# Performance work log

Measured on AMD Instinct MI355X. Metric: run time of the kernel, lower is better.

The kernel has to match this reference:

```python
import jax, jax.numpy as jnp
import numpy as np

B, T, D, H = 8, 512, 1024, 16
DH = D // H  # per-head feature dim (64)


def setup_inputs() -> dict:
    key = jax.random.key(0)
    ks = jax.random.split(key, 10)
    s = 1.0 / np.sqrt(DH)
    inp = {
        "X_data": jax.random.normal(ks[0], (B, T, D), dtype=jnp.float32),
        "mask": jnp.ones((B, T), dtype=jnp.int32),
        # per-head Q/K/V projections (each SelfAttention has its own d_h x d_h weights)
        "Wq": jax.random.normal(ks[1], (H, DH, DH), dtype=jnp.float32) * s,
        "bq": jnp.zeros((H, DH), dtype=jnp.float32),
        "Wk": jax.random.normal(ks[2], (H, DH, DH), dtype=jnp.float32) * s,
        "bk": jnp.zeros((H, DH), dtype=jnp.float32),
        "Wv": jax.random.normal(ks[3], (H, DH, DH), dtype=jnp.float32) * s,
        "bv": jnp.zeros((H, DH), dtype=jnp.float32),
        # AttentionFusion: linear on concatenated head outputs -> len_feature_new
        "Wf": jax.random.normal(ks[4], (D, D), dtype=jnp.float32) * (1.0 / np.sqrt(D)),
        "bf": jnp.zeros((D,), dtype=jnp.float32),
    }
    return inp


def reference(X_data, mask, Wq, bq, Wk, bk, Wv, bv, Wf, bf):
    # Split features into heads: [B, T, H, DH] (equal partitions since D % H == 0)
    Xh = X_data.reshape(B, T, H, DH)
    # Batched per-head projections (replaces the Python loop over heads)
    Q = jnp.einsum("bthd,hde->bhte", Xh, Wq) + bq[None, :, None, :]
    K = jnp.einsum("bthd,hde->bhte", Xh, Wk) + bk[None, :, None, :]
    V = jnp.einsum("bthd,hde->bhte", Xh, Wv) + bv[None, :, None, :]
    scale = 1.0 / jnp.sqrt(jnp.asarray(DH, dtype=Q.dtype))
    scores = jnp.einsum("bhqe,bhke->bhqk", Q, K) * scale  # [B, H, T, T]
    scores = jnp.where(mask[:, None, None, :] > 0, scores, jnp.asarray(-1e9, scores.dtype))
    att = jax.nn.softmax(scores, axis=-1)
    out = jnp.einsum("bhqk,bhke->bhqe", att, V)  # [B, H, T, DH]
    # Concatenate heads (same order as the per-head loop) and fuse
    out = out.transpose(0, 2, 1, 3).reshape(B, T, D)
    fused = out @ Wf + bf  # AttentionFusion linear
    return fused
```

## Files before the change

### kernel.cpp

```cpp
#include <hip/hip_runtime.h>
#include <math.h>

#define B 8
#define T 512
#define D 1024
#define H 16
#define DH 64

typedef __bf16 bf16;
typedef __attribute__((ext_vector_type(8))) __bf16 bf16x8;
typedef __attribute__((ext_vector_type(4))) __bf16 bf16x4;
typedef __attribute__((ext_vector_type(4))) float f32x4;

__device__ __forceinline__ void gld16(const void* g, void* l) {
    __builtin_amdgcn_global_load_lds(
        (const __attribute__((address_space(1))) void*)g,
        (__attribute__((address_space(3))) void*)l, 16, 0, 0);
}


__global__ __launch_bounds__(256) void prep_w(
    const float* __restrict__ Wq, const float* __restrict__ Wk,
    const float* __restrict__ Wv, const float* __restrict__ Wf,
    bf16* __restrict__ WqT, bf16* __restrict__ WkT,
    bf16* __restrict__ WvT, bf16* __restrict__ WfT)
{
    __shared__ bf16 Ts[64 * 72];
    const int blk = blockIdx.x, tid = threadIdx.x;
    if (blk < 48) {
        const int m = blk >> 4, h = blk & 15;
        const float* src = (m == 0 ? Wq : (m == 1 ? Wk : Wv)) + h * 4096;
        bf16* dst = (m == 0 ? WqT : (m == 1 ? WkT : WvT)) + h * 4096;
        for (int i = tid; i < 1024; i += 256) {
            const int d = i >> 4, eq = (i & 15) * 4;
            const float4 w = *(const float4*)(src + d * 64 + eq);
            Ts[(eq + 0) * 72 + d] = (bf16)w.x; Ts[(eq + 1) * 72 + d] = (bf16)w.y;
            Ts[(eq + 2) * 72 + d] = (bf16)w.z; Ts[(eq + 3) * 72 + d] = (bf16)w.w;
        }
        __syncthreads();
        for (int i = tid; i < 512; i += 256) {
            const int e = i >> 3, kc = (i & 7) * 8;
            *(bf16x8*)(dst + e * 64 + kc) = *(const bf16x8*)&Ts[e * 72 + kc];
        }
    } else {
        const int ti = blk - 48, k0 = (ti >> 4) * 64, n0 = (ti & 15) * 64;
        for (int i = tid; i < 1024; i += 256) {
            const int k = i >> 4, nq = (i & 15) * 4;
            const float4 w = *(const float4*)(Wf + (size_t)(k0 + k) * D + n0 + nq);
            Ts[(nq + 0) * 72 + k] = (bf16)w.x; Ts[(nq + 1) * 72 + k] = (bf16)w.y;
            Ts[(nq + 2) * 72 + k] = (bf16)w.z; Ts[(nq + 3) * 72 + k] = (bf16)w.w;
        }
        __syncthreads();
        for (int i = tid; i < 512; i += 256) {
            const int n = i >> 3, kc = (i & 7) * 8;
            *(bf16x8*)(WfT + (size_t)(n0 + n) * D + k0 + kc) = *(const bf16x8*)&Ts[n * 72 + kc];
        }
    }
}

__global__ __launch_bounds__(256) void qkv_mfma(
    const float* __restrict__ X,
    const bf16* __restrict__ WqT, const bf16* __restrict__ WkT,
    const bf16* __restrict__ WvT,
    const float* __restrict__ bq, const float* __restrict__ bk,
    const float* __restrict__ bv,
    bf16* __restrict__ Qb, bf16* __restrict__ Kb, bf16* __restrict__ Vtb)
{
    __shared__ bf16 Xs[128 * 64];
    __shared__ bf16 Wqs[64 * 64], Wks[64 * 64], Wvs[64 * 64];
    __shared__ bf16 Stage[128 * 76];

    const int bh = blockIdx.x & 127, t0 = (blockIdx.x >> 7) * 128;
    const int b = bh >> 4, h = bh & 15;
    const int tid = threadIdx.x, wave = tid >> 6, lane = tid & 63;
    const int quad = lane >> 4, l15 = lane & 15;
    const int lr = lane >> 3, lc = lane & 7;
    const int csw = (lc ^ lr) * 8;

    for (int i = tid; i < 1024; i += 256) {
        const int row = i >> 3, c = i & 7;
        const float* src = X + (size_t)(b * T + t0 + row) * D + h * DH + c * 8;
        const float4 x0 = *(const float4*)src;
        const float4 x1 = *(const float4*)(src + 4);
        bf16x8 t;
        t[0] = (bf16)x0.x; t[1] = (bf16)x0.y; t[2] = (bf16)x0.z; t[3] = (bf16)x0.w;
        t[4] = (bf16)x1.x; t[5] = (bf16)x1.y; t[6] = (bf16)x1.z; t[7] = (bf16)x1.w;
        *(bf16x8*)&Xs[row * 64 + (c ^ (row & 7)) * 8] = t;
    }
    {
        const int r1 = wave * 16;
#pragma unroll
        for (int j = 0; j < 2; ++j) {
            gld16(WqT + (size_t)h * 4096 + (r1 + j * 8 + lr) * 64 + csw, &Wqs[(r1 + j * 8) * 64]);
            gld16(WkT + (size_t)h * 4096 + (r1 + j * 8 + lr) * 64 + csw, &Wks[(r1 + j * 8) * 64]);
            gld16(WvT + (size_t)h * 4096 + (r1 + j * 8 + lr) * 64 + csw, &Wvs[(r1 + j * 8) * 64]);
        }
    }
    __syncthreads();

    bf16x8 af[2][2];
#pragma unroll
    for (int mt = 0; mt < 2; ++mt)
#pragma unroll
        for (int ks = 0; ks < 2; ++ks) {
            const int row = wave * 32 + mt * 16 + l15;
            af[mt][ks] = *(const bf16x8*)&Xs[row * 64 + ((ks * 4 + quad) ^ (l15 & 7)) * 8];
        }

    auto compute = [&](const bf16* Bmat, f32x4 acc[2][4]) {
#pragma unroll
        for (int ks = 0; ks < 2; ++ks) {
            bf16x8 bfr[4];
#pragma unroll
            for (int nt = 0; nt < 4; ++nt)
                bfr[nt] = *(const bf16x8*)&Bmat[(nt * 16 + l15) * 64 + ((ks * 4 + quad) ^ (l15 & 7)) * 8];
#pragma unroll
            for (int mt = 0; mt < 2; ++mt)
#pragma unroll
                for (int nt = 0; nt < 4; ++nt)
                    acc[mt][nt] = __builtin_amdgcn_mfma_f32_16x16x32_bf16(
                        af[mt][ks], bfr[nt], acc[mt][nt], 0, 0, 0);
        }
    };

    const size_t bhTD = (size_t)bh * T * DH;

    {
        f32x4 acc[2][4] = {};
        compute(Wqs, acc);
#pragma unroll
        for (int mt = 0; mt < 2; ++mt)
#pragma unroll
            for (int nt = 0; nt < 4; ++nt) {
                const float bias = bq[h * DH + nt * 16 + l15];
#pragma unroll
                for (int reg = 0; reg < 4; ++reg)
                    Stage[(wave * 32 + mt * 16 + quad * 4 + reg) * 76 + nt * 16 + l15] =
                        (bf16)((acc[mt][nt][reg] + bias) * 0.125f);
            }
        __syncthreads();
        for (int i = tid; i < 1024; i += 256) {
            const int row = i >> 3, c = (i & 7) * 8;
            *(bf16x8*)(Qb + bhTD + (size_t)(t0 + row) * DH + c) = *(const bf16x8*)&Stage[row * 76 + c];
        }
        __syncthreads();
    }
    {
        f32x4 acc[2][4] = {};
        compute(Wks, acc);
#pragma unroll
        for (int mt = 0; mt < 2; ++mt)
#pragma unroll
            for (int nt = 0; nt < 4; ++nt) {
                const float bias = bk[h * DH + nt * 16 + l15];
#pragma unroll
                for (int reg = 0; reg < 4; ++reg)
                    Stage[(wave * 32 + mt * 16 + quad * 4 + reg) * 76 + nt * 16 + l15] =
                        (bf16)(acc[mt][nt][reg] + bias);
            }
        __syncthreads();
        for (int i = tid; i < 1024; i += 256) {
            const int row = i >> 3, c = (i & 7) * 8;
            *(bf16x8*)(Kb + bhTD + (size_t)(t0 + row) * DH + c) = *(const bf16x8*)&Stage[row * 76 + c];
        }
        __syncthreads();
    }
    {
        f32x4 acc[2][4] = {};
        compute(Wvs, acc);
#pragma unroll
        for (int mt = 0; mt < 2; ++mt)
#pragma unroll
            for (int nt = 0; nt < 4; ++nt) {
                const int e = nt * 16 + l15;
                const float bias = bv[h * DH + e];
#pragma unroll
                for (int reg = 0; reg < 4; ++reg) {
                    const int tl = wave * 32 + mt * 16 + quad * 4 + reg;
                    Stage[e * 152 + tl] = (bf16)(acc[mt][nt][reg] + bias);
                }
            }
        __syncthreads();
        for (int i = tid; i < 1024; i += 256) {
            const int e = i >> 4, c = (i & 15) * 8;
            *(bf16x8*)(Vtb + (size_t)bh * DH * T + (size_t)e * T + t0 + c) =
                *(const bf16x8*)&Stage[e * 152 + c];
        }
    }
}

__global__ __launch_bounds__(256) void attn_mfma(
    const bf16* __restrict__ Qb, const bf16* __restrict__ Kb,
    const bf16* __restrict__ Vtb, const int* __restrict__ mask,
    bf16* __restrict__ Ob)
{
    __shared__ bf16 Ks[128 * 64];
    __shared__ bf16 Vts[64 * 128];
    __shared__ bf16 Pl[4][32 * 136];
    __shared__ int msk[128];

    const int bh = blockIdx.x & 127, q0 = (blockIdx.x >> 7) * 128;
    const int b = bh >> 4, h = bh & 15;
    const int tid = threadIdx.x, wave = tid >> 6, lane = tid & 63;
    const int quad = lane >> 4, l15 = lane & 15;
    const int lr = lane >> 3, lc = lane & 7;
    const int csw = (lc ^ lr) * 8;

    const size_t bhTD = (size_t)bh * T * DH;
    const size_t bhDT = (size_t)bh * DH * T;

    bf16x8 qf[2][2];
#pragma unroll
    for (int mt = 0; mt < 2; ++mt)
#pragma unroll
        for (int ks = 0; ks < 2; ++ks)
            qf[mt][ks] = *(const bf16x8*)(Qb + bhTD +
                (size_t)(q0 + wave * 32 + mt * 16 + l15) * DH + ks * 32 + quad * 8);

    f32x4 acc[2][4] = {};
    float lst[2][4] = {};

    for (int kt = 0; kt < 4; ++kt) {
        const int k0 = kt * 128;
        __syncthreads();
        {
            const int r0 = wave * 32;
#pragma unroll
            for (int j = 0; j < 4; ++j)
                gld16(Kb + bhTD + (size_t)(k0 + r0 + j * 8 + lr) * DH + csw,
                      &Ks[(r0 + j * 8) * 64]);
            const int e0 = wave * 16;
#pragma unroll
            for (int j = 0; j < 4; ++j) {
                const int er = j * 4 + (lane >> 4);
                const int csw2 = ((lane & 15) ^ er) * 8;
                gld16(Vtb + bhDT + (size_t)(e0 + er) * T + k0 + csw2,
                      &Vts[(e0 + j * 4) * 128]);
            }
            if (tid < 128) msk[tid] = mask[(size_t)b * T + k0 + tid];
        }
        __syncthreads();

#pragma unroll
        for (int nt = 0; nt < 8; ++nt) {
            const int krow = nt * 16 + l15;
            const bf16x8 kf0 = *(const bf16x8*)&Ks[krow * 64 + ((quad) ^ (l15 & 7)) * 8];
            const bf16x8 kf1 = *(const bf16x8*)&Ks[krow * 64 + ((4 + quad) ^ (l15 & 7)) * 8];
            const int mv = msk[krow];
#pragma unroll
            for (int mt = 0; mt < 2; ++mt) {
                f32x4 s = {};
                s = __builtin_amdgcn_mfma_f32_16x16x32_bf16(qf[mt][0], kf0, s, 0, 0, 0);
                s = __builtin_amdgcn_mfma_f32_16x16x32_bf16(qf[mt][1], kf1, s, 0, 0, 0);
#pragma unroll
                for (int reg = 0; reg < 4; ++reg) {
                    const float p = (mv > 0) ? __expf(s[reg]) : 0.f;
                    lst[mt][reg] += p;
                    Pl[wave][(mt * 16 + quad * 4 + reg) * 136 + nt * 16 + l15] = (bf16)p;
                }
            }
        }
        __builtin_amdgcn_wave_barrier();

#pragma unroll
        for (int kc = 0; kc < 4; ++kc) {
            const bf16x8 pf0 = *(const bf16x8*)&Pl[wave][(l15) * 136 + kc * 32 + quad * 8];
            const bf16x8 pf1 = *(const bf16x8*)&Pl[wave][(16 + l15) * 136 + kc * 32 + quad * 8];
#pragma unroll
            for (int nt = 0; nt < 4; ++nt) {
                const int erow = nt * 16 + l15;
                const bf16x8 vf = *(const bf16x8*)&Vts[erow * 128 + ((kc * 4 + quad) ^ (l15 & 15)) * 8];
                acc[0][nt] = __builtin_amdgcn_mfma_f32_16x16x32_bf16(pf0, vf, acc[0][nt], 0, 0, 0);
                acc[1][nt] = __builtin_amdgcn_mfma_f32_16x16x32_bf16(pf1, vf, acc[1][nt], 0, 0, 0);
            }
        }
    }

    __syncthreads();
    bf16* Ostage = &Pl[0][0];
#pragma unroll
    for (int mt = 0; mt < 2; ++mt)
#pragma unroll
        for (int reg = 0; reg < 4; ++reg) {
            float l = lst[mt][reg];
            l += __shfl_xor(l, 1);
            l += __shfl_xor(l, 2);
            l += __shfl_xor(l, 4);
            l += __shfl_xor(l, 8);
            const float inv = 1.f / l;
            const int row = wave * 32 + mt * 16 + quad * 4 + reg;
#pragma unroll
            for (int nt = 0; nt < 4; ++nt)
                Ostage[row * 76 + nt * 16 + l15] = (bf16)(acc[mt][nt][reg] * inv);
        }
    __syncthreads();
    for (int i = tid; i < 1024; i += 256) {
        const int row = i >> 3, c = (i & 7) * 8;
        *(bf16x8*)(Ob + ((size_t)b * T + q0 + row) * D + h * DH + c) =
            *(const bf16x8*)&Ostage[row * 76 + c];
    }
}

__global__ __launch_bounds__(256) void fuse_mfma(
    const bf16* __restrict__ Ob, const bf16* __restrict__ WfT,
    const float* __restrict__ bfv, float* __restrict__ out)
{
    __shared__ bf16 smem[128 * 128 + 64 * 128];
    bf16* As = smem;
    bf16* Bs = smem + 128 * 128;

    const int col0 = blockIdx.x * 64;
    const int row0 = blockIdx.y * 128;
    const int tid = threadIdx.x, wave = tid >> 6, lane = tid & 63;
    const int quad = lane >> 4, l15 = lane & 15;
    const int lr4 = lane >> 4, lc16 = lane & 15;
    const int wm = wave * 32;

    f32x4 acc[2][4] = {};

    for (int k0 = 0; k0 < D; k0 += 128) {
        __syncthreads();
#pragma unroll
        for (int j = 0; j < 8; ++j) {
            const int row = wm + j * 4 + lr4;
            gld16(Ob + (size_t)(row0 + row) * D + k0 + ((lc16 ^ (row & 15)) * 8),
                  &As[(wm + j * 4) * 128]);
        }
#pragma unroll
        for (int j = 0; j < 4; ++j) {
            const int row = wave * 16 + j * 4 + lr4;
            gld16(WfT + (size_t)(col0 + row) * D + k0 + ((lc16 ^ (row & 15)) * 8),
                  &Bs[(wave * 16 + j * 4) * 128]);
        }
        __syncthreads();
#pragma unroll
        for (int ks = 0; ks < 4; ++ks) {
            bf16x8 af[2], bfr[4];
#pragma unroll
            for (int mt = 0; mt < 2; ++mt) {
                const int row = wm + mt * 16 + l15;
                af[mt] = *(const bf16x8*)&As[row * 128 + ((ks * 4 + quad) ^ l15) * 8];
            }
#pragma unroll
            for (int nt = 0; nt < 4; ++nt)
                bfr[nt] = *(const bf16x8*)&Bs[(nt * 16 + l15) * 128 + ((ks * 4 + quad) ^ l15) * 8];
#pragma unroll
            for (int mt = 0; mt < 2; ++mt)
#pragma unroll
                for (int nt = 0; nt < 4; ++nt)
                    acc[mt][nt] = __builtin_amdgcn_mfma_f32_16x16x32_bf16(af[mt], bfr[nt], acc[mt][nt], 0, 0, 0);
        }
    }

    __syncthreads();
    float* Ofs = (float*)smem;
    float bias[4];
#pragma unroll
    for (int nt = 0; nt < 4; ++nt) bias[nt] = bfv[col0 + nt * 16 + l15];
#pragma unroll
    for (int mt = 0; mt < 2; ++mt)
#pragma unroll
        for (int reg = 0; reg < 4; ++reg) {
            const int row = wm + mt * 16 + quad * 4 + reg;
#pragma unroll
            for (int nt = 0; nt < 4; ++nt)
                Ofs[row * 68 + nt * 16 + l15] = acc[mt][nt][reg] + bias[nt];
        }
    __syncthreads();
    for (int i = tid; i < 2048; i += 256) {
        const int row = i >> 4, c = (i & 15) * 4;
        *(float4*)(out + (size_t)(row0 + row) * D + col0 + c) = *(const float4*)&Ofs[row * 68 + c];
    }
}

extern "C" void kernel_launch(void* const* d_in, const int* in_sizes, int n_in,
                              void* d_out, int out_size, void* d_ws, size_t ws_size,
                              hipStream_t stream) {
    const float* X   = (const float*)d_in[0];
    const int* mask  = (const int*)d_in[1];
    const float* Wq  = (const float*)d_in[2];
    const float* bq  = (const float*)d_in[3];
    const float* Wk  = (const float*)d_in[4];
    const float* bk  = (const float*)d_in[5];
    const float* Wv  = (const float*)d_in[6];
    const float* bv  = (const float*)d_in[7];
    const float* Wf  = (const float*)d_in[8];
    const float* bfv = (const float*)d_in[9];
    float* out = (float*)d_out;

    bf16* wsb = (bf16*)d_ws;
    const size_t QN = (size_t)B * H * T * DH;
    bf16* Qb  = wsb;
    bf16* Kb  = wsb + QN;
    bf16* Vtb = wsb + 2 * QN;
    bf16* Ob  = wsb + 3 * QN;
    bf16* WfT = wsb + 4 * QN;
    bf16* WqT = WfT + (size_t)D * D;
    bf16* WkT = WqT + H * DH * DH;
    bf16* WvT = WkT + H * DH * DH;

    prep_w<<<dim3(304), 256, 0, stream>>>(Wq, Wk, Wv, Wf, WqT, WkT, WvT, WfT);
    qkv_mfma<<<dim3(B * H * 4), 256, 0, stream>>>(X, WqT, WkT, WvT, bq, bk, bv, Qb, Kb, Vtb);
    attn_mfma<<<dim3(B * H * 4), 256, 0, stream>>>(Qb, Kb, Vtb, mask, Ob);
    fuse_mfma<<<dim3(D / 64, (B * T) / 128), 256, 0, stream>>>(Ob, WfT, bfv, out);
}
```

Baseline: 129.3 us.

## Halve per-block tiles in all three kernels to raise block count and occupancy

The QKV, attention and fusion kernels all shrink their row tile from 128 to 64, which doubles the grid to 1024 blocks each and cuts per-wave work to a single 16-row MFMA tile. Shared memory is reduced by aliasing buffers and using smaller tiles, and launch bounds request four blocks per CU. This spreads work across more CUs and hides latency better. In exchange, each loaded K/V and weight tile is reused by fewer rows and there are more block launches. The attention and fusion epilogues now write results directly to global memory instead of staging through LDS for coalesced stores, which may produce less efficient scattered stores.

```diff
diff --git a/kernel.cpp b/kernel.cpp
--- a/kernel.cpp
+++ b/kernel.cpp
@@ -9,7 +9,6 @@
 
 typedef __bf16 bf16;
 typedef __attribute__((ext_vector_type(8))) __bf16 bf16x8;
-typedef __attribute__((ext_vector_type(4))) __bf16 bf16x4;
 typedef __attribute__((ext_vector_type(4))) float f32x4;
 
 __device__ __forceinline__ void gld16(const void* g, void* l) {
@@ -58,7 +57,7 @@
     }
 }
 
-__global__ __launch_bounds__(256) void qkv_mfma(
+__global__ __launch_bounds__(256, 4) void qkv_mfma(
     const float* __restrict__ X,
     const bf16* __restrict__ WqT, const bf16* __restrict__ WkT,
     const bf16* __restrict__ WvT,
@@ -66,18 +65,20 @@
     const float* __restrict__ bv,
     bf16* __restrict__ Qb, bf16* __restrict__ Kb, bf16* __restrict__ Vtb)
 {
-    __shared__ bf16 Xs[128 * 64];
-    __shared__ bf16 Wqs[64 * 64], Wks[64 * 64], Wvs[64 * 64];
-    __shared__ bf16 Stage[128 * 76];
-
-    const int bh = blockIdx.x & 127, t0 = (blockIdx.x >> 7) * 128;
+    __shared__ bf16 RegionA[8192];
+    __shared__ bf16 Wks[64 * 64], Wvs[64 * 64];
+    bf16* Xs = RegionA;
+    bf16* Wqs = RegionA + 4096;
+    bf16* Stage = RegionA;
+
+    const int bh = blockIdx.x & 127, t0 = (blockIdx.x >> 7) * 64;
     const int b = bh >> 4, h = bh & 15;
     const int tid = threadIdx.x, wave = tid >> 6, lane = tid & 63;
     const int quad = lane >> 4, l15 = lane & 15;
     const int lr = lane >> 3, lc = lane & 7;
     const int csw = (lc ^ lr) * 8;
 
-    for (int i = tid; i < 1024; i += 256) {
+    for (int i = tid; i < 512; i += 256) {
         const int row = i >> 3, c = i & 7;
         const float* src = X + (size_t)(b * T + t0 + row) * D + h * DH + c * 8;
         const float4 x0 = *(const float4*)src;
@@ -98,16 +99,14 @@
     }
     __syncthreads();
 
-    bf16x8 af[2][2];
-#pragma unroll
-    for (int mt = 0; mt < 2; ++mt)
-#pragma unroll
-        for (int ks = 0; ks < 2; ++ks) {
-            const int row = wave * 32 + mt * 16 + l15;
-            af[mt][ks] = *(const bf16x8*)&Xs[row * 64 + ((ks * 4 + quad) ^ (l15 & 7)) * 8];
-        }
-
-    auto compute = [&](const bf16* Bmat, f32x4 acc[2][4]) {
+    bf16x8 af[2];
+#pragma unroll
+    for (int ks = 0; ks < 2; ++ks) {
+        const int row = wave * 16 + l15;
+        af[ks] = *(const bf16x8*)&Xs[row * 64 + ((ks * 4 + quad) ^ (l15 & 7)) * 8];
+    }
+
+    auto compute = [&](const bf16* Bmat, f32x4 acc[4]) {
 #pragma unroll
         for (int ks = 0; ks < 2; ++ks) {
             bf16x8 bfr[4];
@@ -115,91 +114,83 @@
             for (int nt = 0; nt < 4; ++nt)
                 bfr[nt] = *(const bf16x8*)&Bmat[(nt * 16 + l15) * 64 + ((ks * 4 + quad) ^ (l15 & 7)) * 8];
 #pragma unroll
-            for (int mt = 0; mt < 2; ++mt)
-#pragma unroll
-                for (int nt = 0; nt < 4; ++nt)
-                    acc[mt][nt] = __builtin_amdgcn_mfma_f32_16x16x32_bf16(
-                        af[mt][ks], bfr[nt], acc[mt][nt], 0, 0, 0);
+            for (int nt = 0; nt < 4; ++nt)
+                acc[nt] = __builtin_amdgcn_mfma_f32_16x16x32_bf16(af[ks], bfr[nt], acc[nt], 0, 0, 0);
         }
     };
 
     const size_t bhTD = (size_t)bh * T * DH;
 
     {
-        f32x4 acc[2][4] = {};
+        f32x4 acc[4] = {};
         compute(Wqs, acc);
-#pragma unroll
-        for (int mt = 0; mt < 2; ++mt)
-#pragma unroll
-            for (int nt = 0; nt < 4; ++nt) {
-                const float bias = bq[h * DH + nt * 16 + l15];
-#pragma unroll
-                for (int reg = 0; reg < 4; ++reg)
-                    Stage[(wave * 32 + mt * 16 + quad * 4 + reg) * 76 + nt * 16 + l15] =
-                        (bf16)((acc[mt][nt][reg] + bias) * 0.125f);
+        __syncthreads();
+#pragma unroll
+        for (int nt = 0; nt < 4; ++nt) {
+            const float bias = bq[h * DH + nt * 16 + l15];
+#pragma unroll
+            for (int reg = 0; reg < 4; ++reg)
+                Stage[(wave * 16 + quad * 4 + reg) * 72 + nt * 16 + l15] =
+                    (bf16)((acc[nt][reg] + bias) * 0.125f);
+        }
+        __syncthreads();
+        for (int i = tid; i < 512; i += 256) {
+            const int row = i >> 3, c = (i & 7) * 8;
+            *(bf16x8*)(Qb + bhTD + (size_t)(t0 + row) * DH + c) = *(const bf16x8*)&Stage[row * 72 + c];
+        }
+        __syncthreads();
+    }
+    {
+        f32x4 acc[4] = {};
+        compute(Wks, acc);
+#pragma unroll
+        for (int nt = 0; nt < 4; ++nt) {
+            const float bias = bk[h * DH + nt * 16 + l15];
+#pragma unroll
+            for (int reg = 0; reg < 4; ++reg)
+                Stage[(wave * 16 + quad * 4 + reg) * 72 + nt * 16 + l15] =
+                    (bf16)(acc[nt][reg] + bias);
+        }
+        __syncthreads();
+        for (int i = tid; i < 512; i += 256) {
+            const int row = i >> 3, c = (i & 7) * 8;
+            *(bf16x8*)(Kb + bhTD + (size_t)(t0 + row) * DH + c) = *(const bf16x8*)&Stage[row * 72 + c];
+        }
+        __syncthreads();
+    }
+    {
+        f32x4 acc[4] = {};
+        compute(Wvs, acc);
+#pragma unroll
+        for (int nt = 0; nt < 4; ++nt) {
+            const int e = nt * 16 + l15;
+            const float bias = bv[h * DH + e];
+#pragma unroll
+            for (int reg = 0; reg < 4; ++reg) {
+                const int tl = wave * 16 + quad * 4 + reg;
+                Stage[e * 72 + tl] = (bf16)(acc[nt][reg] + bias);
             }
-        __syncthreads();
-        for (int i = tid; i < 1024; i += 256) {
-            const int row = i >> 3, c = (i & 7) * 8;
-            *(bf16x8*)(Qb + bhTD + (size_t)(t0 + row) * DH + c) = *(const bf16x8*)&Stage[row * 76 + c];
-        }
-        __syncthreads();
-    }
-    {
-        f32x4 acc[2][4] = {};
-        compute(Wks, acc);
-#pragma unroll
-        for (int mt = 0; mt < 2; ++mt)
-#pragma unroll
-            for (int nt = 0; nt < 4; ++nt) {
-                const float bias = bk[h * DH + nt * 16 + l15];
-#pragma unroll
-                for (int reg = 0; reg < 4; ++reg)
-                    Stage[(wave * 32 + mt * 16 + quad * 4 + reg) * 76 + nt * 16 + l15] =
-                        (bf16)(acc[mt][nt][reg] + bias);
-            }
-        __syncthreads();
-        for (int i = tid; i < 1024; i += 256) {
-            const int row = i >> 3, c = (i & 7) * 8;
-            *(bf16x8*)(Kb + bhTD + (size_t)(t0 + row) * DH + c) = *(const bf16x8*)&Stage[row * 76 + c];
-        }
-        __syncthreads();
-    }
-    {
-        f32x4 acc[2][4] = {};
-        compute(Wvs, acc);
-#pragma unroll
-        for (int mt = 0; mt < 2; ++mt)
-#pragma unroll
-            for (int nt = 0; nt < 4; ++nt) {
-                const int e = nt * 16 + l15;
-                const float bias = bv[h * DH + e];
-#pragma unroll
-                for (int reg = 0; reg < 4; ++reg) {
-                    const int tl = wave * 32 + mt * 16 + quad * 4 + reg;
-                    Stage[e * 152 + tl] = (bf16)(acc[mt][nt][reg] + bias);
-                }
-            }
-        __syncthreads();
-        for (int i = tid; i < 1024; i += 256) {
-            const int e = i >> 4, c = (i & 15) * 8;
+        }
+        __syncthreads();
+        for (int i = tid; i < 512; i += 256) {
+            const int e = i >> 3, c = (i & 7) * 8;
             *(bf16x8*)(Vtb + (size_t)bh * DH * T + (size_t)e * T + t0 + c) =
-                *(const bf16x8*)&Stage[e * 152 + c];
-        }
-    }
-}
-
-__global__ __launch_bounds__(256) void attn_mfma(
+                *(const bf16x8*)&Stage[e * 72 + c];
+        }
+    }
+}
+
+__global__ __launch_bounds__(256, 4) void attn_mfma(
     const bf16* __restrict__ Qb, const bf16* __restrict__ Kb,
     const bf16* __restrict__ Vtb, const int* __restrict__ mask,
     bf16* __restrict__ Ob)
 {
-    __shared__ bf16 Ks[128 * 64];
-    __shared__ bf16 Vts[64 * 128];
-    __shared__ bf16 Pl[4][32 * 136];
-    __shared__ int msk[128];
-
-    const int bh = blockIdx.x & 127, q0 = (blockIdx.x >> 7) * 128;
+    __shared__ bf16 Ks[64 * 64];
+    __shared__ bf16 Vts[64 * 64];
+    __shared__ bf16 Pl[4][16 * 64];
+    __shared__ int msk[64];
+
+    const int bh = blockIdx.x & 127, q0 = (blockIdx.x >> 7) * 64;
     const int b = bh >> 4, h = bh & 15;
     const int tid = threadIdx.x, wave = tid >> 6, lane = tid & 63;
     const int quad = lane >> 4, l15 = lane & 15;
@@ -209,167 +200,123 @@
     const size_t bhTD = (size_t)bh * T * DH;
     const size_t bhDT = (size_t)bh * DH * T;
 
-    bf16x8 qf[2][2];
-#pragma unroll
-    for (int mt = 0; mt < 2; ++mt)
-#pragma unroll
-        for (int ks = 0; ks < 2; ++ks)
-            qf[mt][ks] = *(const bf16x8*)(Qb + bhTD +
-                (size_t)(q0 + wave * 32 + mt * 16 + l15) * DH + ks * 32 + quad * 8);
-
-    f32x4 acc[2][4] = {};
-    float lst[2][4] = {};
-
-    for (int kt = 0; kt < 4; ++kt) {
-        const int k0 = kt * 128;
+    bf16x8 qf[2];
+#pragma unroll
+    for (int ks = 0; ks < 2; ++ks)
+        qf[ks] = *(const bf16x8*)(Qb + bhTD +
+            (size_t)(q0 + wave * 16 + l15) * DH + ks * 32 + quad * 8);
+
+    f32x4 acc[4] = {};
+    float lst[4] = {};
+
+    for (int kt = 0; kt < 8; ++kt) {
+        const int k0 = kt * 64;
         __syncthreads();
         {
-            const int r0 = wave * 32;
-#pragma unroll
-            for (int j = 0; j < 4; ++j)
-                gld16(Kb + bhTD + (size_t)(k0 + r0 + j * 8 + lr) * DH + csw,
-                      &Ks[(r0 + j * 8) * 64]);
-            const int e0 = wave * 16;
-#pragma unroll
-            for (int j = 0; j < 4; ++j) {
-                const int er = j * 4 + (lane >> 4);
-                const int csw2 = ((lane & 15) ^ er) * 8;
-                gld16(Vtb + bhDT + (size_t)(e0 + er) * T + k0 + csw2,
-                      &Vts[(e0 + j * 4) * 128]);
-            }
-            if (tid < 128) msk[tid] = mask[(size_t)b * T + k0 + tid];
-        }
-        __syncthreads();
-
-#pragma unroll
-        for (int nt = 0; nt < 8; ++nt) {
+            const int r0 = wave * 16;
+            gld16(Kb + bhTD + (size_t)(k0 + r0 + lr) * DH + csw, &Ks[r0 * 64]);
+            gld16(Kb + bhTD + (size_t)(k0 + r0 + 8 + lr) * DH + csw, &Ks[(r0 + 8) * 64]);
+            gld16(Vtb + bhDT + (size_t)(r0 + lr) * T + k0 + csw, &Vts[r0 * 64]);
+            gld16(Vtb + bhDT + (size_t)(r0 + 8 + lr) * T + k0 + csw, &Vts[(r0 + 8) * 64]);
+            if (tid < 64) msk[tid] = mask[(size_t)b * T + k0 + tid];
+        }
+        __syncthreads();
+
+#pragma unroll
+        for (int nt = 0; nt < 4; ++nt) {
             const int krow = nt * 16 + l15;
             const bf16x8 kf0 = *(const bf16x8*)&Ks[krow * 64 + ((quad) ^ (l15 & 7)) * 8];
             const bf16x8 kf1 = *(const bf16x8*)&Ks[krow * 64 + ((4 + quad) ^ (l15 & 7)) * 8];
             const int mv = msk[krow];
-#pragma unroll
-            for (int mt = 0; mt < 2; ++mt) {
-                f32x4 s = {};
-                s = __builtin_amdgcn_mfma_f32_16x16x32_bf16(qf[mt][0], kf0, s, 0, 0, 0);
-                s = __builtin_amdgcn_mfma_f32_16x16x32_bf16(qf[mt][1], kf1, s, 0, 0, 0);
-#pragma unroll
-                for (int reg = 0; reg < 4; ++reg) {
-                    const float p = (mv > 0) ? __expf(s[reg]) : 0.f;
-                    lst[mt][reg] += p;
-                    Pl[wave][(mt * 16 + quad * 4 + reg) * 136 + nt * 16 + l15] = (bf16)p;
-                }
+            f32x4 s = {};
+            s = __builtin_amdgcn_mfma_f32_16x16x32_bf16(qf[0], kf0, s, 0, 0, 0);
+            s = __builtin_amdgcn_mfma_f32_16x16x32_bf16(qf[1], kf1, s, 0, 0, 0);
+#pragma unroll
+            for (int reg = 0; reg < 4; ++reg) {
+                const float p = (mv > 0) ? __expf(s[reg]) : 0.f;
+                lst[reg] += p;
+                const int q = quad * 4 + reg;
+                const int c = nt * 2 + (l15 >> 3);
+                Pl[wave][q * 64 + ((c ^ (q & 7)) * 8) + (l15 & 7)] = (bf16)p;
             }
         }
         __builtin_amdgcn_wave_barrier();
 
 #pragma unroll
-        for (int kc = 0; kc < 4; ++kc) {
-            const bf16x8 pf0 = *(const bf16x8*)&Pl[wave][(l15) * 136 + kc * 32 + quad * 8];
-            const bf16x8 pf1 = *(const bf16x8*)&Pl[wave][(16 + l15) * 136 + kc * 32 + quad * 8];
+        for (int kc = 0; kc < 2; ++kc) {
+            const bf16x8 pf = *(const bf16x8*)&Pl[wave][l15 * 64 + (((kc * 4 + quad) ^ (l15 & 7)) * 8)];
 #pragma unroll
             for (int nt = 0; nt < 4; ++nt) {
                 const int erow = nt * 16 + l15;
-                const bf16x8 vf = *(const bf16x8*)&Vts[erow * 128 + ((kc * 4 + quad) ^ (l15 & 15)) * 8];
-                acc[0][nt] = __builtin_amdgcn_mfma_f32_16x16x32_bf16(pf0, vf, acc[0][nt], 0, 0, 0);
-                acc[1][nt] = __builtin_amdgcn_mfma_f32_16x16x32_bf16(pf1, vf, acc[1][nt], 0, 0, 0);
+                const bf16x8 vf = *(const bf16x8*)&Vts[erow * 64 + (((kc * 4 + quad) ^ (l15 & 7)) * 8)];
+                acc[nt] = __builtin_amdgcn_mfma_f32_16x16x32_bf16(pf, vf, acc[nt], 0, 0, 0);
             }
         }
     }
 
-    __syncthreads();
-    bf16* Ostage = &Pl[0][0];
-#pragma unroll
-    for (int mt = 0; mt < 2; ++mt)
-#pragma unroll
-        for (int reg = 0; reg < 4; ++reg) {
-            float l = lst[mt][reg];
-            l += __shfl_xor(l, 1);
-            l += __shfl_xor(l, 2);
-            l += __shfl_xor(l, 4);
-            l += __shfl_xor(l, 8);
-            const float inv = 1.f / l;
-            const int row = wave * 32 + mt * 16 + quad * 4 + reg;
-#pragma unroll
-            for (int nt = 0; nt < 4; ++nt)
-                Ostage[row * 76 + nt * 16 + l15] = (bf16)(acc[mt][nt][reg] * inv);
-        }
-    __syncthreads();
-    for (int i = tid; i < 1024; i += 256) {
-        const int row = i >> 3, c = (i & 7) * 8;
-        *(bf16x8*)(Ob + ((size_t)b * T + q0 + row) * D + h * DH + c) =
-            *(const bf16x8*)&Ostage[row * 76 + c];
-    }
-}
-
-__global__ __launch_bounds__(256) void fuse_mfma(
+#pragma unroll
+    for (int reg = 0; reg < 4; ++reg) {
+        float l = lst[reg];
+        l += __shfl_xor(l, 1);
+        l += __shfl_xor(l, 2);
+        l += __shfl_xor(l, 4);
+        l += __shfl_xor(l, 8);
+        const float inv = 1.f / l;
+        const int t = q0 + wave * 16 + quad * 4 + reg;
+#pragma unroll
+        for (int nt = 0; nt < 4; ++nt)
+            Ob[((size_t)b * T + t) * D + h * DH + nt * 16 + l15] =
+                (bf16)(acc[nt][reg] * inv);
+    }
+}
+
+__global__ __launch_bounds__(256, 4) void fuse_mfma(
     const bf16* __restrict__ Ob, const bf16* __restrict__ WfT,
     const float* __restrict__ bfv, float* __restrict__ out)
 {
-    __shared__ bf16 smem[128 * 128 + 64 * 128];
-    bf16* As = smem;
-    bf16* Bs = smem + 128 * 128;
+    __shared__ bf16 As[64 * 128];
+    __shared__ bf16 Bs[64 * 128];
 
     const int col0 = blockIdx.x * 64;
-    const int row0 = blockIdx.y * 128;
+    const int row0 = blockIdx.y * 64;
     const int tid = threadIdx.x, wave = tid >> 6, lane = tid & 63;
     const int quad = lane >> 4, l15 = lane & 15;
     const int lr4 = lane >> 4, lc16 = lane & 15;
-    const int wm = wave * 32;
-
-    f32x4 acc[2][4] = {};
+
+    f32x4 acc[4] = {};
 
     for (int k0 = 0; k0 < D; k0 += 128) {
         __syncthreads();
-#pragma unroll
-        for (int j = 0; j < 8; ++j) {
-            const int row = wm + j * 4 + lr4;
-            gld16(Ob + (size_t)(row0 + row) * D + k0 + ((lc16 ^ (row & 15)) * 8),
-                  &As[(wm + j * 4) * 128]);
-        }
 #pragma unroll
         for (int j = 0; j < 4; ++j) {
             const int row = wave * 16 + j * 4 + lr4;
-            gld16(WfT + (size_t)(col0 + row) * D + k0 + ((lc16 ^ (row & 15)) * 8),
-                  &Bs[(wave * 16 + j * 4) * 128]);
+            const int cs = (lc16 ^ (row & 15)) * 8;
+            gld16(Ob + (size_t)(row0 + row) * D + k0 + cs, &As[(wave * 16 + j * 4) * 128]);
+            gld16(WfT + (size_t)(col0 + row) * D + k0 + cs, &Bs[(wave * 16 + j * 4) * 128]);
         }
         __syncthreads();
 #pragma unroll
         for (int ks = 0; ks < 4; ++ks) {
-            bf16x8 af[2], bfr[4];
-#pragma unroll
-            for (int mt = 0; mt < 2; ++mt) {
-                const int row = wm + mt * 16 + l15;
-                af[mt] = *(const bf16x8*)&As[row * 128 + ((ks * 4 + quad) ^ l15) * 8];
+            const int arow = wave * 16 + l15;
+            const bf16x8 af = *(const bf16x8*)&As[arow * 128 + ((ks * 4 + quad) ^ (arow & 15)) * 8];
+#pragma unroll
+            for (int nt = 0; nt < 4; ++nt) {
+                const int brow = nt * 16 + l15;
+                const bf16x8 bfr = *(const bf16x8*)&Bs[brow * 128 + ((ks * 4 + quad) ^ (brow & 15)) * 8];
+                acc[nt] = __builtin_amdgcn_mfma_f32_16x16x32_bf16(af, bfr, acc[nt], 0, 0, 0);
             }
-#pragma unroll
-            for (int nt = 0; nt < 4; ++nt)
-                bfr[nt] = *(const bf16x8*)&Bs[(nt * 16 + l15) * 128 + ((ks * 4 + quad) ^ l15) * 8];
-#pragma unroll
-            for (int mt = 0; mt < 2; ++mt)
-#pragma unroll
-                for (int nt = 0; nt < 4; ++nt)
-                    acc[mt][nt] = __builtin_amdgcn_mfma_f32_16x16x32_bf16(af[mt], bfr[nt], acc[mt][nt], 0, 0, 0);
-        }
-    }
-
-    __syncthreads();
-    float* Ofs = (float*)smem;
+        }
+    }
+
     float bias[4];
 #pragma unroll
     for (int nt = 0; nt < 4; ++nt) bias[nt] = bfv[col0 + nt * 16 + l15];
 #pragma unroll
-    for (int mt = 0; mt < 2; ++mt)
-#pragma unroll
-        for (int reg = 0; reg < 4; ++reg) {
-            const int row = wm + mt * 16 + quad * 4 + reg;
-#pragma unroll
-            for (int nt = 0; nt < 4; ++nt)
-                Ofs[row * 68 + nt * 16 + l15] = acc[mt][nt][reg] + bias[nt];
-        }
-    __syncthreads();
-    for (int i = tid; i < 2048; i += 256) {
-        const int row = i >> 4, c = (i & 15) * 4;
-        *(float4*)(out + (size_t)(row0 + row) * D + col0 + c) = *(const float4*)&Ofs[row * 68 + c];
+    for (int reg = 0; reg < 4; ++reg) {
+        const int r = row0 + wave * 16 + quad * 4 + reg;
+#pragma unroll
+        for (int nt = 0; nt < 4; ++nt)
+            out[(size_t)r * D + col0 + nt * 16 + l15] = acc[nt][reg] + bias[nt];
     }
 }
 
@@ -400,7 +347,7 @@
     bf16* WvT = WkT + H * DH * DH;
 
     prep_w<<<dim3(304), 256, 0, stream>>>(Wq, Wk, Wv, Wf, WqT, WkT, WvT, WfT);
-    qkv_mfma<<<dim3(B * H * 4), 256, 0, stream>>>(X, WqT, WkT, WvT, bq, bk, bv, Qb, Kb, Vtb);
-    attn_mfma<<<dim3(B * H * 4), 256, 0, stream>>>(Qb, Kb, Vtb, mask, Ob);
-    fuse_mfma<<<dim3(D / 64, (B * T) / 128), 256, 0, stream>>>(Ob, WfT, bfv, out);
-}
+    qkv_mfma<<<dim3(1024), 256, 0, stream>>>(X, WqT, WkT, WvT, bq, bk, bv, Qb, Kb, Vtb);
+    attn_mfma<<<dim3(1024), 256, 0, stream>>>(Qb, Kb, Vtb, mask, Ob);
+    fuse_mfma<<<dim3(16, 64), 256, 0, stream>>>(Ob, WfT, bfv, out);
+}
```

After: 130.6 us. No clear change (+1.0%).

## Merge four kernels into one cooperative persistent kernel with grid syncs

Applied to the files above, without the earlier changes.

Folds the weight-prep, QKV projection, attention and output-fusion kernels into one cooperative kernel of 512 blocks. The phases share one statically allocated shared-memory buffer and are separated by grid-wide barriers. The aim is to remove three kernel launch gaps and the tail idle time between launches. In exchange, every phase waits on a full grid barrier and shared-memory use is fixed at the largest phase's size, which may cut occupancy. If the cooperative launch fails, it falls back to four separate kernels.

```diff
diff --git a/kernel.cpp b/kernel.cpp
--- a/kernel.cpp
+++ b/kernel.cpp
@@ -1,5 +1,8 @@
 #include <hip/hip_runtime.h>
+#include <hip/hip_cooperative_groups.h>
 #include <math.h>
+
+namespace cg = cooperative_groups;
 
 #define B 8
 #define T 512
@@ -9,7 +12,6 @@
 
 typedef __bf16 bf16;
 typedef __attribute__((ext_vector_type(8))) __bf16 bf16x8;
-typedef __attribute__((ext_vector_type(4))) __bf16 bf16x4;
 typedef __attribute__((ext_vector_type(4))) float f32x4;
 
 __device__ __forceinline__ void gld16(const void* g, void* l) {
@@ -19,14 +21,14 @@
 }
 
 
-__global__ __launch_bounds__(256) void prep_w(
+__device__ __forceinline__ void phase_prep(char* smem, int blk, int tid,
     const float* __restrict__ Wq, const float* __restrict__ Wk,
     const float* __restrict__ Wv, const float* __restrict__ Wf,
     bf16* __restrict__ WqT, bf16* __restrict__ WkT,
     bf16* __restrict__ WvT, bf16* __restrict__ WfT)
 {
-    __shared__ bf16 Ts[64 * 72];
-    const int blk = blockIdx.x, tid = threadIdx.x;
+    if (blk >= 304) return;
+    bf16* Ts = (bf16*)smem;
     if (blk < 48) {
         const int m = blk >> 4, h = blk & 15;
         const float* src = (m == 0 ? Wq : (m == 1 ? Wk : Wv)) + h * 4096;
@@ -58,7 +60,7 @@
     }
 }
 
-__global__ __launch_bounds__(256) void qkv_mfma(
+__device__ __forceinline__ void phase_qkv(char* smem, int blk, int tid,
     const float* __restrict__ X,
     const bf16* __restrict__ WqT, const bf16* __restrict__ WkT,
     const bf16* __restrict__ WvT,
@@ -66,13 +68,15 @@
     const float* __restrict__ bv,
     bf16* __restrict__ Qb, bf16* __restrict__ Kb, bf16* __restrict__ Vtb)
 {
-    __shared__ bf16 Xs[128 * 64];
-    __shared__ bf16 Wqs[64 * 64], Wks[64 * 64], Wvs[64 * 64];
-    __shared__ bf16 Stage[128 * 76];
-
-    const int bh = blockIdx.x & 127, t0 = (blockIdx.x >> 7) * 128;
+    bf16* Xs    = (bf16*)smem;
+    bf16* Wqs   = (bf16*)(smem + 16384);
+    bf16* Wks   = (bf16*)(smem + 24576);
+    bf16* Wvs   = (bf16*)(smem + 32768);
+    bf16* Stage = (bf16*)(smem + 40960);
+
+    const int bh = blk & 127, t0 = (blk >> 7) * 128;
     const int b = bh >> 4, h = bh & 15;
-    const int tid = threadIdx.x, wave = tid >> 6, lane = tid & 63;
+    const int wave = tid >> 6, lane = tid & 63;
     const int quad = lane >> 4, l15 = lane & 15;
     const int lr = lane >> 3, lc = lane & 7;
     const int csw = (lc ^ lr) * 8;
@@ -189,25 +193,26 @@
     }
 }
 
-__global__ __launch_bounds__(256) void attn_mfma(
+__device__ __forceinline__ void phase_attn(char* smem, int blk, int tid,
     const bf16* __restrict__ Qb, const bf16* __restrict__ Kb,
     const bf16* __restrict__ Vtb, const int* __restrict__ mask,
     bf16* __restrict__ Ob)
 {
-    __shared__ bf16 Ks[128 * 64];
-    __shared__ bf16 Vts[64 * 128];
-    __shared__ bf16 Pl[4][32 * 136];
-    __shared__ int msk[128];
-
-    const int bh = blockIdx.x & 127, q0 = (blockIdx.x >> 7) * 128;
+    bf16* Ks  = (bf16*)smem;
+    bf16* Vts = (bf16*)(smem + 16384);
+    bf16* Pl  = (bf16*)(smem + 32768);
+    int*  msk = (int*)(smem + 67584);
+
+    const int bh = blk & 127, q0 = (blk >> 7) * 128;
     const int b = bh >> 4, h = bh & 15;
-    const int tid = threadIdx.x, wave = tid >> 6, lane = tid & 63;
+    const int wave = tid >> 6, lane = tid & 63;
     const int quad = lane >> 4, l15 = lane & 15;
     const int lr = lane >> 3, lc = lane & 7;
     const int csw = (lc ^ lr) * 8;
 
     const size_t bhTD = (size_t)bh * T * DH;
     const size_t bhDT = (size_t)bh * DH * T;
+    bf16* Plw = Pl + wave * (32 * 136);
 
     bf16x8 qf[2][2];
 #pragma unroll
@@ -256,7 +261,7 @@
                 for (int reg = 0; reg < 4; ++reg) {
                     const float p = (mv > 0) ? __expf(s[reg]) : 0.f;
                     lst[mt][reg] += p;
-                    Pl[wave][(mt * 16 + quad * 4 + reg) * 136 + nt * 16 + l15] = (bf16)p;
+                    Plw[(mt * 16 + quad * 4 + reg) * 136 + nt * 16 + l15] = (bf16)p;
                 }
             }
         }
@@ -264,8 +269,8 @@
 
 #pragma unroll
         for (int kc = 0; kc < 4; ++kc) {
-            const bf16x8 pf0 = *(const bf16x8*)&Pl[wave][(l15) * 136 + kc * 32 + quad * 8];
-            const bf16x8 pf1 = *(const bf16x8*)&Pl[wave][(16 + l15) * 136 + kc * 32 + quad * 8];
+            const bf16x8 pf0 = *(const bf16x8*)&Plw[(l15) * 136 + kc * 32 + quad * 8];
+            const bf16x8 pf1 = *(const bf16x8*)&Plw[(16 + l15) * 136 + kc * 32 + quad * 8];
 #pragma unroll
             for (int nt = 0; nt < 4; ++nt) {
                 const int erow = nt * 16 + l15;
@@ -277,7 +282,7 @@
     }
 
     __syncthreads();
-    bf16* Ostage = &Pl[0][0];
+    bf16* Ostage = Pl;
 #pragma unroll
     for (int mt = 0; mt < 2; ++mt)
 #pragma unroll
@@ -301,17 +306,16 @@
     }
 }
 
-__global__ __launch_bounds__(256) void fuse_mfma(
+__device__ __forceinline__ void phase_fuse(char* smem, int blk, int tid,
     const bf16* __restrict__ Ob, const bf16* __restrict__ WfT,
     const float* __restrict__ bfv, float* __restrict__ out)
 {
-    __shared__ bf16 smem[128 * 128 + 64 * 128];
-    bf16* As = smem;
-    bf16* Bs = smem + 128 * 128;
-
-    const int col0 = blockIdx.x * 64;
-    const int row0 = blockIdx.y * 128;
-    const int tid = threadIdx.x, wave = tid >> 6, lane = tid & 63;
+    bf16* As = (bf16*)smem;
+    bf16* Bs = (bf16*)(smem + 32768);
+
+    const int col0 = (blk & 15) * 64;
+    const int row0 = (blk >> 4) * 128;
+    const int wave = tid >> 6, lane = tid & 63;
     const int quad = lane >> 4, l15 = lane & 15;
     const int lr4 = lane >> 4, lc16 = lane & 15;
     const int wm = wave * 32;
@@ -371,6 +375,57 @@
         const int row = i >> 4, c = (i & 15) * 4;
         *(float4*)(out + (size_t)(row0 + row) * D + col0 + c) = *(const float4*)&Ofs[row * 68 + c];
     }
+}
+
+__global__ __launch_bounds__(256, 2) void mha_mega(
+    const float* X, const int* mask,
+    const float* Wq, const float* bq, const float* Wk, const float* bk,
+    const float* Wv, const float* bv, const float* Wf, const float* bfv,
+    bf16* Qb, bf16* Kb, bf16* Vtb, bf16* Ob,
+    bf16* WqT, bf16* WkT, bf16* WvT, bf16* WfT, float* out)
+{
+    __shared__ __align__(16) char smem[68608];
+    const int blk = blockIdx.x, tid = threadIdx.x;
+    cg::grid_group grid = cg::this_grid();
+
+    phase_prep(smem, blk, tid, Wq, Wk, Wv, Wf, WqT, WkT, WvT, WfT);
+    __threadfence();
+    grid.sync();
+    phase_qkv(smem, blk, tid, X, WqT, WkT, WvT, bq, bk, bv, Qb, Kb, Vtb);
+    __threadfence();
+    grid.sync();
+    phase_attn(smem, blk, tid, Qb, Kb, Vtb, mask, Ob);
+    __threadfence();
+    grid.sync();
+    phase_fuse(smem, blk, tid, Ob, WfT, bfv, out);
+}
+
+__global__ __launch_bounds__(256) void k_prep(
+    const float* Wq, const float* Wk, const float* Wv, const float* Wf,
+    bf16* WqT, bf16* WkT, bf16* WvT, bf16* WfT)
+{
+    __shared__ __align__(16) char smem[9216];
+    phase_prep(smem, blockIdx.x, threadIdx.x, Wq, Wk, Wv, Wf, WqT, WkT, WvT, WfT);
+}
+__global__ __launch_bounds__(256, 2) void k_qkv(
+    const float* X, const bf16* WqT, const bf16* WkT, const bf16* WvT,
+    const float* bq, const float* bk, const float* bv,
+    bf16* Qb, bf16* Kb, bf16* Vtb)
+{
+    __shared__ __align__(16) char smem[60416];
+    phase_qkv(smem, blockIdx.x, threadIdx.x, X, WqT, WkT, WvT, bq, bk, bv, Qb, Kb, Vtb);
+}
+__global__ __launch_bounds__(256, 2) void k_attn(
+    const bf16* Qb, const bf16* Kb, const bf16* Vtb, const int* mask, bf16* Ob)
+{
+    __shared__ __align__(16) char smem[68608];
+    phase_attn(smem, blockIdx.x, threadIdx.x, Qb, Kb, Vtb, mask, Ob);
+}
+__global__ __launch_bounds__(256, 2) void k_fuse(
+    const bf16* Ob, const bf16* WfT, const float* bfv, float* out)
+{
+    __shared__ __align__(16) char smem[49152];
+    phase_fuse(smem, blockIdx.x, threadIdx.x, Ob, WfT, bfv, out);
 }
 
 extern "C" void kernel_launch(void* const* d_in, const int* in_sizes, int n_in,
@@ -399,8 +454,19 @@
     bf16* WkT = WqT + H * DH * DH;
     bf16* WvT = WkT + H * DH * DH;
 
-    prep_w<<<dim3(304), 256, 0, stream>>>(Wq, Wk, Wv, Wf, WqT, WkT, WvT, WfT);
-    qkv_mfma<<<dim3(B * H * 4), 256, 0, stream>>>(X, WqT, WkT, WvT, bq, bk, bv, Qb, Kb, Vtb);
-    attn_mfma<<<dim3(B * H * 4), 256, 0, stream>>>(Qb, Kb, Vtb, mask, Ob);
-    fuse_mfma<<<dim3(D / 64, (B * T) / 128), 256, 0, stream>>>(Ob, WfT, bfv, out);
-}
+    void* args[] = { (void*)&X, (void*)&mask, (void*)&Wq, (void*)&bq,
+                     (void*)&Wk, (void*)&bk, (void*)&Wv, (void*)&bv,
+                     (void*)&Wf, (void*)&bfv, (void*)&Qb, (void*)&Kb,
+                     (void*)&Vtb, (void*)&Ob, (void*)&WqT, (void*)&WkT,
+                     (void*)&WvT, (void*)&WfT, (void*)&out };
+    hipError_t e = hipLaunchCooperativeKernel((const void*)mha_mega,
+                                              dim3(512), dim3(256),
+                                              args, 0, stream);
+    if (e != hipSuccess) {
+        (void)hipGetLastError();
+        k_prep<<<dim3(304), 256, 0, stream>>>(Wq, Wk, Wv, Wf, WqT, WkT, WvT, WfT);
+        k_qkv<<<dim3(512), 256, 0, stream>>>(X, WqT, WkT, WvT, bq, bk, bv, Qb, Kb, Vtb);
+        k_attn<<<dim3(512), 256, 0, stream>>>(Qb, Kb, Vtb, mask, Ob);
+        k_fuse<<<dim3(512), 256, 0, stream>>>(Ob, WfT, bfv, out);
+    }
+}
```

After: 463.5 us. 3.58x slower.
